# Kernel optimization log

Measured on AMD Instinct MI355X. Metric: run time of the kernel, lower is better.

## Reference

```python
import jax, jax.numpy as jnp
import numpy as np

NUM_BBOX = 2
NUM_CLASSES = 20
NUM_GRID = 7
THR_CONF = 0.5
THR_NMS = 0.3
BATCH = 128


def setup_inputs() -> dict:
    key = jax.random.key(0)
    C = NUM_BBOX * 4 + NUM_BBOX + NUM_CLASSES  # 30
    p = jax.random.normal(key, (BATCH, NUM_GRID, NUM_GRID, C), dtype=jnp.float32)
    return {"p_yolo_ts4": p}


def _decode(p):
    B, S = p.shape[0], p.shape[1]
    sc = NUM_BBOX * 4
    conf = jax.nn.sigmoid(p[..., sc:sc + NUM_BBOX])          # [B,S,S,nb] objectness
    cls = jax.nn.sigmoid(p[..., sc + NUM_BBOX:])             # [B,S,S,nc]
    boxes = p[..., :sc].reshape(B, S, S, NUM_BBOX, 4)
    xy = jax.nn.sigmoid(boxes[..., :2])                      # cell-relative offsets
    col = jnp.arange(S, dtype=p.dtype)
    cx = (xy[..., 0] + col[None, None, :, None]) / NUM_GRID  # + col index (x)
    cy = (xy[..., 1] + col[None, :, None, None]) / NUM_GRID  # + row index (y)
    w, h = boxes[..., 2], boxes[..., 3]                      # raw wh, as in source
    ltrb = jnp.stack([cx - w / 2, cy - h / 2, cx + w / 2, cy + h / 2], axis=-1)
    labels = jnp.argmax(cls, axis=-1) + 1                    # [B,S,S]
    valid = conf > THR_CONF                                  # [B,S,S,nb]
    return ltrb, conf, labels, valid


def _pairwise_iou(b):
    lt = jnp.maximum(b[:, None, :2], b[None, :, :2])
    rb = jnp.minimum(b[:, None, 2:], b[None, :, 2:])
    wh = jnp.clip(rb - lt, 0.0)
    inter = wh[..., 0] * wh[..., 1]
    area = (b[:, 2] - b[:, 0]) * (b[:, 3] - b[:, 1])
    union = area[:, None] + area[None, :] - inter
    return inter / jnp.maximum(union, 1e-9)


def reference(p_yolo_ts4):
    p = p_yolo_ts4
    B, S = p.shape[0], p.shape[1]
    ltrb, conf, labels, valid = _decode(p)
    N = B * S * S * NUM_BBOX
    boxes = ltrb.reshape(N, 4)
    scores = conf.reshape(N)
    labs = jnp.broadcast_to(labels[..., None], (B, S, S, NUM_BBOX)).reshape(N)
    idsb = jnp.broadcast_to(jnp.arange(B)[:, None, None, None], (B, S, S, NUM_BBOX)).reshape(N)
    vmask = valid.reshape(N)
    # sort by score (invalid last); greedy NMS per (batch, label) group
    order = jnp.argsort(jnp.where(vmask, scores, -jnp.inf))[::-1]
    boxes_s = boxes[order]
    scores_s = scores[order]
    labs_s = labs[order]
    idsb_s = idsb[order]
    v_s = vmask[order]
    iou = _pairwise_iou(boxes_s)                              # [N,N]
    same = (idsb_s[:, None] == idsb_s[None, :]) & (labs_s[:, None] == labs_s[None, :])
    later = jnp.arange(N)[None, :] > jnp.arange(N)[:, None]
    sup_mat = (iou > THR_NMS) & same & later & v_s[None, :]

    def body(i, sup):
        keep_i = v_s[i] & jnp.logical_not(sup[i])
        return jnp.where(keep_i, sup | sup_mat[i], sup)

    sup = jax.lax.fori_loop(0, N, body, jnp.zeros((N,), dtype=bool))
    keep = v_s & jnp.logical_not(sup)
    # fixed-shape outputs in descending-score order; `keep` marks surviving boxes
    return idsb_s, boxes_s, labs_s, scores_s, keep
```

## Files before the change

### kernel.cpp

```cpp
#include <hip/hip_runtime.h>
#include <math.h>

#define NBATCH 128
#define S 7
#define CH 30
#define N 12544
#define PERB 98
#define NCH 16
#define CLEN 784
#define THRNMS 0.3

__device__ __forceinline__ float sigf(float x) {
    float e = (float)exp(-(double)x);
    return 1.0f / (1.0f + e);
}

__global__ __launch_bounds__(256) void k_decode(
    const float* __restrict__ p,
    unsigned long long* __restrict__ K,
    float4* __restrict__ box4,
    float* __restrict__ score,
    int* __restrict__ meta)
{
    int i    = blockIdx.x * 256 + threadIdx.x;
    int j    = i & 1;
    int cell = i >> 1;
    int x = cell % S, y = (cell / S) % S;
    const float* pc = p + cell * CH;

    float tx = pc[j*4+0], ty = pc[j*4+1], tw = pc[j*4+2], th = pc[j*4+3];
    float craw = pc[8 + j];

    int cbase = 10 + j * 10;
    float best = sigf(pc[cbase]); int lab = j * 10;
    #pragma unroll
    for (int c = 1; c < 10; ++c) {
        float v = sigf(pc[cbase + c]);
        if (v > best) { best = v; lab = j * 10 + c; }
    }
    float obest = __shfl_xor(best, 1);
    int   olab  = __shfl_xor(lab, 1);
    float bestA = j ? obest : best;  int labA = j ? olab : lab;
    float bestB = j ? best  : obest; int labB = j ? lab  : olab;
    int label = (bestB > bestA ? labB : labA) + 1;

    float sx = sigf(tx), sy = sigf(ty);
    float cx = (sx + (float)x) / 7.0f;
    float cy = (sy + (float)y) / 7.0f;
    float hw = tw / 2.0f, hh = th / 2.0f;
    float l = cx - hw, t = cy - hh, r = cx + hw, bt = cy + hh;

    float sc = sigf(craw);
    bool valid = sc > 0.5f;

    K[i] = valid ? (((unsigned long long)__float_as_uint(sc) << 32)
                    | (unsigned long long)(unsigned int)i)
                 : (unsigned long long)(unsigned int)i;
    box4[i]  = make_float4(l, t, r, bt);
    score[i] = sc;
    meta[i]  = label;
}

__global__ __launch_bounds__(256) void k_rank(
    const unsigned long long* __restrict__ K,
    unsigned int* __restrict__ vpart)
{
    __shared__ unsigned long long lk[CLEN];
    const int tid = threadIdx.x;
    const unsigned int base = blockIdx.y * CLEN;

    for (int u = tid; u < CLEN; u += 256) lk[u] = K[base + u];
    __syncthreads();

    const unsigned int row = blockIdx.x * 256 + tid;
    const unsigned long long Ki = K[row];
    unsigned int cnt = 0;
    #pragma unroll 8
    for (int u = 0; u < CLEN; ++u)
        cnt += (lk[u] > Ki) ? 1u : 0u;
    vpart[blockIdx.y * N + row] = cnt;
}

__global__ __launch_bounds__(128) void k_finish(
    const unsigned long long* __restrict__ K,
    const float4* __restrict__ box4,
    const float* __restrict__ score,
    const int* __restrict__ meta,
    const unsigned int* __restrict__ vpart,
    float* __restrict__ out)
{
    const int b = blockIdx.x, tid = threadIdx.x;
    __shared__ unsigned long long Ka[PERB];
    __shared__ float bxa[PERB][4];
    __shared__ float sca[PERB];
    __shared__ int   laba[PERB];
    __shared__ unsigned int posa[PERB];
    __shared__ int   srk[PERB];
    __shared__ float sbx[PERB][4];
    __shared__ int   slb[PERB], sup[PERB];
    __shared__ unsigned int kb_sh;

    if (tid == 0) kb_sh = 0u;
    __syncthreads();

    if (tid < PERB) {
        int i = b * PERB + tid;
        unsigned long long Kt = K[i];
        Ka[tid] = Kt;
        float4 v = box4[i];
        bxa[tid][0] = v.x; bxa[tid][1] = v.y; bxa[tid][2] = v.z; bxa[tid][3] = v.w;
        sca[tid]  = score[i];
        laba[tid] = meta[i];
        unsigned int acc = 0;
        #pragma unroll
        for (int ch = 0; ch < NCH; ++ch) acc += vpart[ch * N + i];
        posa[tid] = acc;
        if (Kt >> 32) atomicAdd(&kb_sh, 1u);
    }
    __syncthreads();
    const int kb = (int)kb_sh;

    if (tid < PERB && (Ka[tid] >> 32)) {
        unsigned long long Kt = Ka[tid];
        int rk = 0;
        for (int u = 0; u < PERB; ++u)
            rk += (Ka[u] > Kt) ? 1 : 0;
        srk[tid] = rk;
        sbx[rk][0] = bxa[tid][0]; sbx[rk][1] = bxa[tid][1];
        sbx[rk][2] = bxa[tid][2]; sbx[rk][3] = bxa[tid][3];
        slb[rk] = laba[tid];
        sup[rk] = 0;
    }
    __syncthreads();

    for (int i = 0; i < kb; ++i) {
        __syncthreads();
        if (sup[i]) continue;
        float li = sbx[i][0], ti = sbx[i][1], ri = sbx[i][2], bi = sbx[i][3];
        float areai = (ri - li) * (bi - ti);
        int labi = slb[i];
        int jj = tid;
        if (jj > i && jj < kb && slb[jj] == labi) {
            float lj = sbx[jj][0], tj = sbx[jj][1], rj = sbx[jj][2], bj = sbx[jj][3];
            float lt0 = fmaxf(li, lj), lt1 = fmaxf(ti, tj);
            float rb0 = fminf(ri, rj), rb1 = fminf(bi, bj);
            float w = rb0 - lt0; if (w < 0.0f) w = 0.0f;
            float h = rb1 - lt1; if (h < 0.0f) h = 0.0f;
            float inter = w * h;
            float areaj = (rj - lj) * (bj - tj);
            float uni = areai + areaj - inter;
            double iou = (double)inter / fmax((double)uni, 1e-9);
            if (iou > THRNMS) sup[jj] = 1;
        }
    }
    __syncthreads();

    if (tid < PERB) {
        unsigned int pos = posa[tid];
        bool valid = (Ka[tid] >> 32) != 0ull;
        out[pos] = (float)b;
        ((float4*)(out + N))[pos] =
            make_float4(bxa[tid][0], bxa[tid][1], bxa[tid][2], bxa[tid][3]);
        out[5*N + pos] = (float)laba[tid];
        out[6*N + pos] = sca[tid];
        out[7*N + pos] = (valid && !sup[srk[tid]]) ? 1.0f : 0.0f;
    }
}

extern "C" void kernel_launch(void* const* d_in, const int* in_sizes, int n_in,
                              void* d_out, int out_size, void* d_ws, size_t ws_size,
                              hipStream_t stream)
{
    const float* p = (const float*)d_in[0];
    float* out = (float*)d_out;

    char* w = (char*)d_ws;
    float4* box4        = (float4*)w;                     w += (size_t)N * 16;
    unsigned long long* K = (unsigned long long*)w;       w += (size_t)N * 8;
    float* score        = (float*)w;                      w += (size_t)N * 4;
    int* meta           = (int*)w;                        w += (size_t)N * 4;
    unsigned int* vpart = (unsigned int*)w;               w += (size_t)NCH * N * 4;

    k_decode<<<dim3(N / 256),   dim3(256), 0, stream>>>(p, K, box4, score, meta);
    k_rank  <<<dim3(49, NCH),   dim3(256), 0, stream>>>(K, vpart);
    k_finish<<<dim3(NBATCH),    dim3(128), 0, stream>>>(K, box4, score, meta, vpart, out);
}
```

Measured before the change: 89.31 us.

## Fuse global ranking into per-batch NMS kernel with compacted valid keys

Removes the separate all-pairs rank kernel and its partial-count buffer. Each per-batch block of 1024 threads compacts the valid keys into shared memory in two halves and counts only against those. Invalid entries get their position from a closed form: the valid count plus the reverse index, corrected by a count of valid entries with larger index. The NMS loop now holds suppression flags as wavefront ballot bitmasks in registers instead of a shared array with a barrier per iteration. In exchange, every block rescans all global keys, so that work is repeated 128 times instead of being spread across blocks.

```diff
diff --git a/kernel.cpp b/kernel.cpp
--- a/kernel.cpp
+++ b/kernel.cpp
@@ -6,8 +6,7 @@
 #define CH 30
 #define N 12544
 #define PERB 98
-#define NCH 16
-#define CLEN 784
+#define HALF 6272
 #define THRNMS 0.3
 
 __device__ __forceinline__ float sigf(float x) {
@@ -61,109 +60,138 @@
     meta[i]  = label;
 }
 
-__global__ __launch_bounds__(256) void k_rank(
-    const unsigned long long* __restrict__ K,
-    unsigned int* __restrict__ vpart)
-{
-    __shared__ unsigned long long lk[CLEN];
-    const int tid = threadIdx.x;
-    const unsigned int base = blockIdx.y * CLEN;
-
-    for (int u = tid; u < CLEN; u += 256) lk[u] = K[base + u];
-    __syncthreads();
-
-    const unsigned int row = blockIdx.x * 256 + tid;
-    const unsigned long long Ki = K[row];
-    unsigned int cnt = 0;
-    #pragma unroll 8
-    for (int u = 0; u < CLEN; ++u)
-        cnt += (lk[u] > Ki) ? 1u : 0u;
-    vpart[blockIdx.y * N + row] = cnt;
-}
-
-__global__ __launch_bounds__(128) void k_finish(
+__global__ __launch_bounds__(1024) void k_batch(
     const unsigned long long* __restrict__ K,
     const float4* __restrict__ box4,
     const float* __restrict__ score,
     const int* __restrict__ meta,
-    const unsigned int* __restrict__ vpart,
     float* __restrict__ out)
 {
-    const int b = blockIdx.x, tid = threadIdx.x;
+    const int b = blockIdx.x, tid = threadIdx.x, lane = tid & 63;
+    __shared__ unsigned long long lk[HALF];
     __shared__ unsigned long long Ka[PERB];
     __shared__ float bxa[PERB][4];
     __shared__ float sca[PERB];
     __shared__ int   laba[PERB];
-    __shared__ unsigned int posa[PERB];
-    __shared__ int   srk[PERB];
+    __shared__ unsigned int rc1[PERB], rc2[PERB];
     __shared__ float sbx[PERB][4];
-    __shared__ int   slb[PERB], sup[PERB];
-    __shared__ unsigned int kb_sh;
-
-    if (tid == 0) kb_sh = 0u;
-    __syncthreads();
-
+    __shared__ int   slb[PERB], srk[PERB];
+    __shared__ unsigned int cnt_sh, nv_sh, kb_sh;
+
+    if (tid == 0) { nv_sh = 0u; kb_sh = 0u; }
     if (tid < PERB) {
+        rc1[tid] = 0u; rc2[tid] = 0u;
         int i = b * PERB + tid;
-        unsigned long long Kt = K[i];
-        Ka[tid] = Kt;
+        Ka[tid] = K[i];
         float4 v = box4[i];
         bxa[tid][0] = v.x; bxa[tid][1] = v.y; bxa[tid][2] = v.z; bxa[tid][3] = v.w;
         sca[tid]  = score[i];
         laba[tid] = meta[i];
-        unsigned int acc = 0;
-        #pragma unroll
-        for (int ch = 0; ch < NCH; ++ch) acc += vpart[ch * N + i];
-        posa[tid] = acc;
-        if (Kt >> 32) atomicAdd(&kb_sh, 1u);
     }
     __syncthreads();
-    const int kb = (int)kb_sh;
-
-    if (tid < PERB && (Ka[tid] >> 32)) {
+
+    for (int h = 0; h < 2; ++h) {
+        if (tid == 0) cnt_sh = 0u;
+        __syncthreads();
+        for (int u = tid; u < HALF; u += 1024) {
+            unsigned long long Kv = K[h * HALF + u];
+            bool valid = (Kv >> 32) != 0ull;
+            unsigned long long bal = __ballot(valid);
+            unsigned int wbase = 0;
+            if (lane == 0) wbase = atomicAdd(&cnt_sh, (unsigned int)__popcll(bal));
+            wbase = __shfl(wbase, 0);
+            if (valid)
+                lk[wbase + __popcll(bal & ((1ull << lane) - 1ull))] = Kv;
+        }
+        __syncthreads();
+        const unsigned int len = cnt_sh;
+        if (tid == 0) nv_sh += len;
+        if (tid < 980) {
+            int row = tid / 10, part = tid - row * 10;
+            unsigned long long Ki = Ka[row];
+            unsigned int ui = (unsigned int)(b * PERB + row);
+            unsigned int c1 = 0, c2 = 0;
+            for (unsigned int u = (unsigned int)part; u < len; u += 10) {
+                unsigned long long Kj = lk[u];
+                c1 += (Kj > Ki) ? 1u : 0u;
+                c2 += ((unsigned int)Kj > ui) ? 1u : 0u;
+            }
+            if (c1) atomicAdd(&rc1[row], c1);
+            if (c2) atomicAdd(&rc2[row], c2);
+        }
+        __syncthreads();
+    }
+    const unsigned int nv = nv_sh;
+
+    const bool own = tid < PERB;
+    const bool validown = own && (Ka[tid] >> 32) != 0ull;
+    if (validown) {
         unsigned long long Kt = Ka[tid];
         int rk = 0;
-        for (int u = 0; u < PERB; ++u)
-            rk += (Ka[u] > Kt) ? 1 : 0;
+        for (int u = 0; u < PERB; ++u) rk += (Ka[u] > Kt) ? 1 : 0;
         srk[tid] = rk;
         sbx[rk][0] = bxa[tid][0]; sbx[rk][1] = bxa[tid][1];
         sbx[rk][2] = bxa[tid][2]; sbx[rk][3] = bxa[tid][3];
         slb[rk] = laba[tid];
-        sup[rk] = 0;
+        atomicAdd(&kb_sh, 1u);
     }
     __syncthreads();
-
+    const int kb = (int)kb_sh;
+
+    int j1 = lane, j2 = lane + 64;
+    float l1=0,t1=0,r1=0,q1=0,a1=0; int lb1 = -1;
+    if (j1 < kb) { l1=sbx[j1][0]; t1=sbx[j1][1]; r1=sbx[j1][2]; q1=sbx[j1][3];
+                   lb1=slb[j1]; a1=(r1-l1)*(q1-t1); }
+    float l2=0,t2=0,r2=0,q2=0,a2=0; int lb2 = -1;
+    if (j2 < kb) { l2=sbx[j2][0]; t2=sbx[j2][1]; r2=sbx[j2][2]; q2=sbx[j2][3];
+                   lb2=slb[j2]; a2=(r2-l2)*(q2-t2); }
+    unsigned long long sup0 = 0ull, sup1 = 0ull;
     for (int i = 0; i < kb; ++i) {
-        __syncthreads();
-        if (sup[i]) continue;
+        bool supi = (i < 64) ? ((sup0 >> i) & 1ull) : ((sup1 >> (i - 64)) & 1ull);
+        if (supi) continue;
         float li = sbx[i][0], ti = sbx[i][1], ri = sbx[i][2], bi = sbx[i][3];
         float areai = (ri - li) * (bi - ti);
         int labi = slb[i];
-        int jj = tid;
-        if (jj > i && jj < kb && slb[jj] == labi) {
-            float lj = sbx[jj][0], tj = sbx[jj][1], rj = sbx[jj][2], bj = sbx[jj][3];
-            float lt0 = fmaxf(li, lj), lt1 = fmaxf(ti, tj);
-            float rb0 = fminf(ri, rj), rb1 = fminf(bi, bj);
+        bool c1b = false, c2b = false;
+        if (j1 > i && j1 < kb && lb1 == labi) {
+            float lt0 = fmaxf(li, l1), lt1 = fmaxf(ti, t1);
+            float rb0 = fminf(ri, r1), rb1 = fminf(bi, q1);
             float w = rb0 - lt0; if (w < 0.0f) w = 0.0f;
-            float h = rb1 - lt1; if (h < 0.0f) h = 0.0f;
-            float inter = w * h;
-            float areaj = (rj - lj) * (bj - tj);
-            float uni = areai + areaj - inter;
-            double iou = (double)inter / fmax((double)uni, 1e-9);
-            if (iou > THRNMS) sup[jj] = 1;
-        }
-    }
-    __syncthreads();
-
-    if (tid < PERB) {
-        unsigned int pos = posa[tid];
-        bool valid = (Ka[tid] >> 32) != 0ull;
+            float hgt = rb1 - lt1; if (hgt < 0.0f) hgt = 0.0f;
+            float inter = w * hgt;
+            float uni = areai + a1 - inter;
+            c1b = ((double)inter / fmax((double)uni, 1e-9)) > THRNMS;
+        }
+        if (j2 > i && j2 < kb && lb2 == labi) {
+            float lt0 = fmaxf(li, l2), lt1 = fmaxf(ti, t2);
+            float rb0 = fminf(ri, r2), rb1 = fminf(bi, q2);
+            float w = rb0 - lt0; if (w < 0.0f) w = 0.0f;
+            float hgt = rb1 - lt1; if (hgt < 0.0f) hgt = 0.0f;
+            float inter = w * hgt;
+            float uni = areai + a2 - inter;
+            c2b = ((double)inter / fmax((double)uni, 1e-9)) > THRNMS;
+        }
+        sup0 |= __ballot(c1b);
+        sup1 |= __ballot(c2b);
+    }
+
+    if (own) {
+        int i = b * PERB + tid;
+        unsigned int pos = validown
+            ? rc1[tid]
+            : nv + (unsigned int)(N - 1 - i) - rc2[tid];
         out[pos] = (float)b;
         ((float4*)(out + N))[pos] =
             make_float4(bxa[tid][0], bxa[tid][1], bxa[tid][2], bxa[tid][3]);
         out[5*N + pos] = (float)laba[tid];
         out[6*N + pos] = sca[tid];
-        out[7*N + pos] = (valid && !sup[srk[tid]]) ? 1.0f : 0.0f;
+        float keep = 0.0f;
+        if (validown) {
+            int m = srk[tid];
+            bool s = (m < 64) ? ((sup0 >> m) & 1ull) : ((sup1 >> (m - 64)) & 1ull);
+            keep = s ? 0.0f : 1.0f;
+        }
+        out[7*N + pos] = keep;
     }
 }
 
@@ -175,13 +203,11 @@
     float* out = (float*)d_out;
 
     char* w = (char*)d_ws;
-    float4* box4        = (float4*)w;                     w += (size_t)N * 16;
-    unsigned long long* K = (unsigned long long*)w;       w += (size_t)N * 8;
-    float* score        = (float*)w;                      w += (size_t)N * 4;
-    int* meta           = (int*)w;                        w += (size_t)N * 4;
-    unsigned int* vpart = (unsigned int*)w;               w += (size_t)NCH * N * 4;
-
-    k_decode<<<dim3(N / 256),   dim3(256), 0, stream>>>(p, K, box4, score, meta);
-    k_rank  <<<dim3(49, NCH),   dim3(256), 0, stream>>>(K, vpart);
-    k_finish<<<dim3(NBATCH),    dim3(128), 0, stream>>>(K, box4, score, meta, vpart, out);
-}
+    float4* box4          = (float4*)w;               w += (size_t)N * 16;
+    unsigned long long* K = (unsigned long long*)w;   w += (size_t)N * 8;
+    float* score          = (float*)w;                w += (size_t)N * 4;
+    int* meta             = (int*)w;                  w += (size_t)N * 4;
+
+    k_decode<<<dim3(N / 256), dim3(256),  0, stream>>>(p, K, box4, score, meta);
+    k_batch <<<dim3(NBATCH),  dim3(1024), 0, stream>>>(K, box4, score, meta, out);
+}
```

After: 120.7 us. +35.1%, slower.
